# Performance work log

Measured on AMD Instinct MI355X. Metric: run time of the kernel, lower is better.

## Reference

```python
import jax, jax.numpy as jnp
from jax import lax
import numpy as np

SLOPE = 0.01   # torch nn.LeakyReLU default
EPS = 1e-5     # BN eps
DN = ('NCDHW', 'OIDHW', 'NCDHW')


def conv3d(x, w, pad):
    return lax.conv_general_dilated(x, w, (1, 1, 1), pad, dimension_numbers=DN)


def bn(x, g, b):
    # BatchNorm1d over all active points == per-channel stats over (N, D, H, W)
    m = jnp.mean(x, axis=(0, 2, 3, 4), keepdims=True)
    v = jnp.var(x, axis=(0, 2, 3, 4), keepdims=True)
    return (x - m) * lax.rsqrt(v + EPS) * g.reshape(1, -1, 1, 1, 1) + b.reshape(1, -1, 1, 1, 1)


def lrelu(x):
    return jnp.where(x >= 0, x, SLOPE * x)


def setup_inputs() -> dict:
    key = jax.random.key(0)
    ks = jax.random.split(key, 8)
    Cin, Cout = 128, 64
    x = jax.random.normal(ks[0], (1, Cin, 16, 48, 48), jnp.float32)      # coarse sparse grid (all-active)
    skip = jax.random.normal(ks[1], (1, Cout, 32, 96, 96), jnp.float32)  # fine skip grid
    s = lambda k, shape, fan: jax.random.normal(k, shape, jnp.float32) * np.float32(1.0 / np.sqrt(fan))
    w_trans = s(ks[2], (Cout, Cin, 3, 3, 3), Cin * 27)
    w_up = s(ks[3], (Cout, Cout, 3, 3, 3), Cout * 27)
    w1 = s(ks[4], (Cout, Cout, 1, 3, 3), Cout * 9)
    w2 = s(ks[5], (Cout, Cout, 3, 1, 3), Cout * 9)
    w3 = s(ks[6], (Cout, Cout, 3, 3, 3), Cout * 27)
    g = jnp.ones((Cout,), jnp.float32)
    b = jnp.zeros((Cout,), jnp.float32)
    return dict(x=x, skip=skip, w_trans=w_trans, g_t=g, b_t=b, w_up=w_up,
                w1=w1, g1=g, b1=b, w2=w2, g2=g, b2=b, w3=w3, g3=g, b3=b)


def reference(x, skip, w_trans, g_t, b_t, w_up, w1, g1, b1, w2, g2, b2, w3, g3, b3):
    # trans_conv (subm 3x3x3) -> LeakyReLU -> BN
    xt = bn(lrelu(conv3d(x, w_trans, [(1, 1)] * 3)), g_t, b_t)
    up = lax.conv_general_dilated(xt, w_up, (1, 1, 1), [(1, 2)] * 3,
                                  lhs_dilation=(2, 2, 2), dimension_numbers=DN)
    up = up + skip
    up = bn(lrelu(conv3d(up, w1, [(0, 0), (1, 1), (1, 1)])), g1, b1)  # conv1x3 (1,3,3)
    up = bn(lrelu(conv3d(up, w2, [(1, 1), (0, 0), (1, 1)])), g2, b2)  # conv3x1 (3,1,3)
    up = bn(lrelu(conv3d(up, w3, [(1, 1)] * 3)), g3, b3)              # conv3x3 (3,3,3)
    return up
```

## Files before the change

### kernel.cpp

```cpp
#include <hip/hip_runtime.h>

#define SLOPE 0.01f
#define BN_EPS 1e-5f

typedef __attribute__((ext_vector_type(8))) short short8;
typedef __attribute__((ext_vector_type(4))) float f32x4;

static constexpr int D1 = 32, H1 = 96, W1_ = 96;
static constexpr int HW1 = H1 * W1_, DHW1 = D1 * HW1;
static constexpr int D0 = 16, H0 = 48, W0 = 48;
static constexpr int HW0 = H0 * W0, DHW0 = D0 * HW0;

static constexpr int FP_PLPTS = 98 * 98;
static constexpr int CP_PLPTS = 50 * 50;
static constexpr int FP_ELEMS = 33 * FP_PLPTS * 64;

__device__ __forceinline__ short f2bf(float f) {
    unsigned u = __builtin_bit_cast(unsigned, f);
    unsigned r = (u + 0x7fffu + ((u >> 16) & 1u)) >> 16;
    return (short)r;
}
__device__ __forceinline__ float bf2f(short s) {
    unsigned u = ((unsigned)(unsigned short)s) << 16;
    return __builtin_bit_cast(float, u);
}
__device__ __forceinline__ int pidx_fine(int s) {
    int z = s / HW1; int r = s - z * HW1; int y = r / W1_; int x = r - y * W1_;
    return z * FP_PLPTS + (y + 1) * 98 + (x + 1);
}
__device__ __forceinline__ int pidx_coarse(int s) {
    int z = s / HW0; int r = s - z * HW0; int y = r / W0; int x = r - y * W0;
    return z * CP_PLPTS + (y + 1) * 50 + (x + 1);
}
__device__ __forceinline__ void gload16(const void* g, void* l) {
    __builtin_amdgcn_global_load_lds(
        (const __attribute__((address_space(1))) void*)g,
        (__attribute__((address_space(3))) void*)l, 16, 0, 0);
}

__global__ __launch_bounds__(256)
void to_cl_pad128(const float* __restrict__ in, short* __restrict__ out)
{
    __shared__ float t[64][65];
    const int s0 = blockIdx.x * 64, c0 = blockIdx.y * 64;
    const int tid = threadIdx.x;
    {
        const int cpr = tid >> 2, ch = tid & 3;
        const float4* ip = (const float4*)(in + (size_t)(c0 + cpr) * DHW0 + s0 + ch * 16);
        #pragma unroll
        for (int i = 0; i < 4; ++i) {
            float4 v = ip[i]; int sb = ch * 16 + i * 4;
            t[sb][cpr] = v.x; t[sb + 1][cpr] = v.y; t[sb + 2][cpr] = v.z; t[sb + 3][cpr] = v.w;
        }
    }
    __syncthreads();
    {
        const int spr = tid >> 2, cc = (tid & 3) * 16;
        short8 o0, o1;
        #pragma unroll
        for (int q = 0; q < 8; ++q) { o0[q] = f2bf(t[spr][cc + q]); o1[q] = f2bf(t[spr][cc + 8 + q]); }
        const int p = pidx_coarse(s0 + spr);
        short* op = out + (size_t)p * 128 + c0 + cc;
        *(short8*)op = o0;
        *(short8*)(op + 8) = o1;
    }
}

__global__ __launch_bounds__(256)
void to_cl_bf16(const float* __restrict__ in, short* __restrict__ out, int S)
{
    __shared__ float t[64][65];
    const int s0 = blockIdx.x * 64;
    const int tid = threadIdx.x;
    {
        const int cpr = tid >> 2, ch = tid & 3;
        const float4* ip = (const float4*)(in + (size_t)cpr * S + s0 + ch * 16);
        #pragma unroll
        for (int i = 0; i < 4; ++i) {
            float4 v = ip[i]; int sb = ch * 16 + i * 4;
            t[sb][cpr] = v.x; t[sb + 1][cpr] = v.y; t[sb + 2][cpr] = v.z; t[sb + 3][cpr] = v.w;
        }
    }
    __syncthreads();
    {
        const int spr = tid >> 2, cc = (tid & 3) * 16;
        short8 o0, o1;
        #pragma unroll
        for (int q = 0; q < 8; ++q) { o0[q] = f2bf(t[spr][cc + q]); o1[q] = f2bf(t[spr][cc + 8 + q]); }
        short* op = out + (size_t)(s0 + spr) * 64 + cc;
        *(short8*)op = o0;
        *(short8*)(op + 8) = o1;
    }
}

__global__ __launch_bounds__(256)
void prep_w(const float* __restrict__ w, short* __restrict__ dst, int CIN, int KSZ)
{
    int i = blockIdx.x * 256 + threadIdx.x;
    int n = KSZ * 64 * CIN;
    if (i >= n) return;
    int t = i / (64 * CIN); int r = i % (64 * CIN); int o = r / CIN; int ci = r % CIN;
    dst[i] = f2bf(w[(size_t)(o * CIN + ci) * KSZ + t]);
}

__global__ void finalize_stats(const float* __restrict__ stats, const float* __restrict__ g,
                               const float* __restrict__ b, float invN, float* __restrict__ aff)
{
    int c = threadIdx.x;
    float m = stats[c] * invN;
    float var = stats[64 + c] * invN - m * m;
    float rstd = rsqrtf(var + BN_EPS);
    float sc = g[c] * rstd;
    aff[c] = sc;
    aff[64 + c] = b[c] - m * sc;
}

template<int MODE>
__global__ __launch_bounds__(256)
void affine_pad(short* __restrict__ buf, const float* __restrict__ aff, int n8)
{
    int i = blockIdx.x * 256 + threadIdx.x;
    if (i >= n8) return;
    int s = i >> 3, cb = (i & 7) * 8;
    int p = (MODE == 1) ? pidx_fine(s) : pidx_coarse(s);
    short* ptr = buf + (size_t)p * 64 + cb;
    short8 v = *(const short8*)ptr;
    short8 o;
    #pragma unroll
    for (int q = 0; q < 8; ++q) {
        int c = cb + q;
        o[q] = f2bf(bf2f(v[q]) * aff[c] + aff[64 + c]);
    }
    *(short8*)ptr = o;
}

__global__ __launch_bounds__(256)
void final_out(const short* __restrict__ in, float* __restrict__ out, const float* __restrict__ aff)
{
    __shared__ float t[64][65];
    const int s0 = blockIdx.x * 64;
    const int tid = threadIdx.x;
    {
        const int spr = tid >> 2, ch = tid & 3;
        const short8* ip = (const short8*)(in + (size_t)(s0 + spr) * 64 + ch * 16);
        short8 v0 = ip[0], v1 = ip[1];
        #pragma unroll
        for (int q = 0; q < 8; ++q) { int c = ch * 16 + q;     t[spr][c] = bf2f(v0[q]) * aff[c] + aff[64 + c]; }
        #pragma unroll
        for (int q = 0; q < 8; ++q) { int c = ch * 16 + 8 + q; t[spr][c] = bf2f(v1[q]) * aff[c] + aff[64 + c]; }
    }
    __syncthreads();
    {
        const int c = tid >> 2, sc = (tid & 3) * 16;
        #pragma unroll
        for (int i = 0; i < 4; ++i) {
            float4 w;
            w.x = t[sc + 4 * i][c]; w.y = t[sc + 4 * i + 1][c];
            w.z = t[sc + 4 * i + 2][c]; w.w = t[sc + 4 * i + 3][c];
            *(float4*)(out + (size_t)c * DHW1 + s0 + sc + 4 * i) = w;
        }
    }
}

template<int GH, int GW, int CIN>
__global__ __launch_bounds__(256)
void zero_halo(short* __restrict__ buf)
{
    constexpr int PPW = GW + 2, PLP = (GH + 2) * PPW, CPR = CIN / 8;
    constexpr int NCHK = (2 * PPW + 2 * GH) * CPR;
    const int pl = blockIdx.x;
    const short8 z8 = {0, 0, 0, 0, 0, 0, 0, 0};
    for (int i = threadIdx.x; i < NCHK; i += 256) {
        int p = i / CPR, c = i % CPR;
        int y, x;
        if (p < PPW) { y = 0; x = p; }
        else if (p < 2 * PPW) { y = GH + 1; x = p - PPW; }
        else { int q = p - 2 * PPW; y = 1 + (q >> 1); x = (q & 1) ? (GW + 1) : 0; }
        *(short8*)(buf + ((size_t)pl * PLP + y * PPW + x) * CIN + c * 8) = z8;
    }
}

template<int MG, int CIN, int KD, int KH, int KW, int PD, int PH, int PW,
         int GD, int GH, int GW, int OUTMODE, bool STATS>
__global__ __launch_bounds__(256, 2)
void convmm5(const short* __restrict__ A, const short* __restrict__ Wt,
             short* __restrict__ Out, float* __restrict__ stats)
{
    constexpr int MR   = 64 * MG;
    constexpr int KSZ  = KD * KH * KW;
    constexpr int PPW  = GW + 2;
    constexpr int PLP  = (GH + 2) * PPW;
    constexpr int HWg  = GH * GW;
    constexpr int CPR  = CIN / 8;
    constexpr int L2C  = (CIN == 64) ? 3 : 4;
    constexpr int RPI  = 64 / CPR;
    constexpr int ASZ  = MR * CIN * 2;
    constexpr int BSZ  = 64 * CIN * 2;
    constexpr int API  = ASZ / 4096;
    constexpr int BPI  = BSZ / 4096;
    constexpr int KCN  = CIN / 32;
    constexpr int S_IF = API + BPI;

    __shared__ char smem[2 * ASZ + 2 * BSZ];

    const int tid = threadIdx.x, lane = tid & 63, wave = tid >> 6;
    const int rl = lane & 15, kg = lane >> 4;

    const int nwg = gridDim.x;
    const int bid = blockIdx.x;
    const int bswz = (nwg & 7) ? bid : ((bid & 7) * (nwg >> 3) + (bid >> 3));
    const int row0 = bswz * MR;

    int zA[API], yxA[API], cofA[API];
    #pragma unroll
    for (int i = 0; i < API; ++i) {
        const int gi = wave * API + i;
        const int r = gi * RPI + (lane >> L2C);
        const int s = row0 + r;
        const int z = s / HWg; const int rm = s - z * HWg;
        const int y = rm / GW; const int x = rm - y * GW;
        zA[i] = z;
        yxA[i] = (y + 1) * PPW + (x + 1);
        cofA[i] = ((lane & (CPR - 1)) ^ (r & 7)) * 8;
    }
    int rB[BPI], cofB[BPI];
    #pragma unroll
    for (int i = 0; i < BPI; ++i) {
        const int gi = wave * BPI + i;
        const int r = gi * RPI + (lane >> L2C);
        rB[i] = r;
        cofB[i] = ((lane & (CPR - 1)) ^ (r & 7)) * 8;
    }

    auto stageA = [&](int bsel, int kd, int kh, int kw) {
        const int dyx = (kh - PH) * PPW + (kw - PW);
        #pragma unroll
        for (int i = 0; i < API; ++i) {
            int zp = zA[i] + (kd - PD);
            int pl = ((unsigned)zp < (unsigned)GD) ? zp : GD;
            const short* src = A + ((size_t)pl * PLP + yxA[i] + dyx) * CIN + cofA[i];
            void* dst = smem + bsel * ASZ + (wave * API + i) * 1024;
            gload16(src, dst);
        }
    };
    auto stageB = [&](int bsel, int t) {
        const short* wt = Wt + (size_t)t * 64 * CIN;
        #pragma unroll
        for (int i = 0; i < BPI; ++i) {
            const short* src = wt + rB[i] * CIN + cofB[i];
            void* dst = smem + 2 * ASZ + bsel * BSZ + (wave * BPI + i) * 1024;
            gload16(src, dst);
        }
    };

    f32x4 acc[MG][4];
    #pragma unroll
    for (int mg = 0; mg < MG; ++mg)
        #pragma unroll
        for (int ng = 0; ng < 4; ++ng)
            acc[mg][ng] = (f32x4){0.f, 0.f, 0.f, 0.f};

    auto comp = [&](int bsel) {
        const short* ab = (const short*)(smem + bsel * ASZ);
        const short* bb = (const short*)(smem + 2 * ASZ + bsel * BSZ);
        #pragma unroll
        for (int kc = 0; kc < KCN; ++kc) {
            short8 av[MG], bv[4];
            #pragma unroll
            for (int mg = 0; mg < MG; ++mg) {
                const int r = wave * (16 * MG) + mg * 16 + rl;
                const int c = (kc * 4 + kg) ^ (r & 7);
                av[mg] = *(const short8*)(ab + r * CIN + c * 8);
            }
            #pragma unroll
            for (int ng = 0; ng < 4; ++ng) {
                const int r = ng * 16 + rl;
                const int c = (kc * 4 + kg) ^ (r & 7);
                bv[ng] = *(const short8*)(bb + r * CIN + c * 8);
            }
            __builtin_amdgcn_s_setprio(1);
            #pragma unroll
            for (int mg = 0; mg < MG; ++mg)
                #pragma unroll
                for (int ng = 0; ng < 4; ++ng)
                    acc[mg][ng] = __builtin_amdgcn_mfma_f32_16x16x32_bf16(av[mg], bv[ng], acc[mg][ng], 0, 0, 0);
            __builtin_amdgcn_s_setprio(0);
        }
    };

    stageA(0, 0, 0, 0);
    stageB(0, 0);

    #pragma unroll
    for (int t = 0; t < KSZ; ++t) {
        const int cur = t & 1;
        if (t + 1 < KSZ) {
            const int t1 = t + 1;
            const int kd = t1 / (KH * KW), rm = t1 % (KH * KW);
            stageA(cur ^ 1, kd, rm / KW, rm % KW);
            stageB(cur ^ 1, t1);
            asm volatile("s_waitcnt vmcnt(%0)" :: "i"(S_IF) : "memory");
        } else {
            asm volatile("s_waitcnt vmcnt(0)" ::: "memory");
        }
        __builtin_amdgcn_s_barrier();
        __builtin_amdgcn_sched_barrier(0);
        comp(cur);
        asm volatile("s_waitcnt lgkmcnt(0)" ::: "memory");
        __builtin_amdgcn_sched_barrier(0);
        __builtin_amdgcn_s_barrier();
    }

    short (*tile)[64] = (short(*)[64])smem;
    float* red = (float*)(smem + 2 * ASZ);

    #pragma unroll
    for (int mg = 0; mg < MG; ++mg)
        #pragma unroll
        for (int ng = 0; ng < 4; ++ng)
            #pragma unroll
            for (int j = 0; j < 4; ++j) {
                float v = acc[mg][ng][j];
                if (STATS) v = (v >= 0.f) ? v : SLOPE * v;
                tile[wave * (16 * MG) + mg * 16 + kg * 4 + j][ng * 16 + rl] = f2bf(v);
            }
    __syncthreads();

    #pragma unroll
    for (int i = 0; i < MR / 32; ++i) {
        const int chunk = i * 256 + tid;
        const int r = chunk >> 3, cc = (chunk & 7) * 8;
        const int s = row0 + r;
        size_t o;
        if (OUTMODE == 0)      o = (size_t)s * 64 + cc;
        else if (OUTMODE == 1) o = (size_t)pidx_fine(s) * 64 + cc;
        else                   o = (size_t)pidx_coarse(s) * 64 + cc;
        *(short8*)(Out + o) = *(const short8*)&tile[r][cc];
    }

    if (STATS) {
        float s1 = 0.f, s2 = 0.f;
        const int col = tid & 63, rg = tid >> 6;
        #pragma unroll 4
        for (int r = rg * (MR / 4); r < (rg + 1) * (MR / 4); ++r) {
            float v = bf2f(tile[r][col]); s1 += v; s2 += v * v;
        }
        red[(0 * 4 + rg) * 64 + col] = s1;
        red[(1 * 4 + rg) * 64 + col] = s2;
        __syncthreads();
        if (tid < 64) {
            float a = red[0 * 256 + 0 * 64 + tid] + red[0 * 256 + 1 * 64 + tid] +
                      red[0 * 256 + 2 * 64 + tid] + red[0 * 256 + 3 * 64 + tid];
            float b = red[1 * 256 + 0 * 64 + tid] + red[1 * 256 + 1 * 64 + tid] +
                      red[1 * 256 + 2 * 64 + tid] + red[1 * 256 + 3 * 64 + tid];
            atomicAdd(&stats[tid], a);
            atomicAdd(&stats[64 + tid], b);
        }
    }
}

__global__ __launch_bounds__(256, 2)
void tconv_cls(const short* __restrict__ Y, const short* __restrict__ Wt,
               const short* __restrict__ SK, short* __restrict__ Out)
{
    const int cls = blockIdx.y;
    const int pz = (cls >> 2) & 1, py = (cls >> 1) & 1, px = cls & 1;
    const int tid = threadIdx.x, lane = tid & 63, wave = tid >> 6;
    const int rl = lane & 15, kg = lane >> 4;
    const int row0 = blockIdx.x * 256;

    int zin0[4], zin1[4];
    #pragma unroll
    for (int mg = 0; mg < 4; ++mg) {
        int s = row0 + wave * 64 + mg * 16 + rl;
        int zc = s / HW0; int r = s - zc * HW0; int yc = r / W0; int xc = r - yc * W0;
        int ib = ((yc + 1) * 50 + (xc + 1)) * 64 + kg * 8;
        zin0[mg] = zc * (CP_PLPTS * 64) + ib;
        zin1[mg] = ((zc + 1 < 16) ? zc + 1 : 16) * (CP_PLPTS * 64) + ib;
    }
    const int boff = rl * 64 + kg * 8;

    f32x4 acc[4][4];
    #pragma unroll
    for (int mg = 0; mg < 4; ++mg)
        #pragma unroll
        for (int ng = 0; ng < 4; ++ng)
            acc[mg][ng] = (f32x4){0.f, 0.f, 0.f, 0.f};

    for (int a = 0; a <= pz; ++a) {
        const int kd = pz ? 2 * a : 1;
        for (int b = 0; b <= py; ++b) {
            const int kh = py ? 2 * b : 1;
            for (int c = 0; c <= px; ++c) {
                const int kw = px ? 2 * c : 1;
                const int t = kd * 9 + kh * 3 + kw;
                const int dlt = (b * 50 + c) * 64;
                int ao[4];
                #pragma unroll
                for (int mg = 0; mg < 4; ++mg)
                    ao[mg] = (a ? zin1[mg] : zin0[mg]) + dlt;
                #pragma unroll
                for (int kc = 0; kc < 2; ++kc) {
                    short8 av[4], bv[4];
                    #pragma unroll
                    for (int mg = 0; mg < 4; ++mg)
                        av[mg] = *(const short8*)(Y + ao[mg] + kc * 32);
                    #pragma unroll
                    for (int ng = 0; ng < 4; ++ng)
                        bv[ng] = *(const short8*)(Wt + (t * 64 + ng * 16) * 64 + boff + kc * 32);
                    #pragma unroll
                    for (int mg = 0; mg < 4; ++mg)
                        #pragma unroll
                        for (int ng = 0; ng < 4; ++ng)
                            acc[mg][ng] = __builtin_amdgcn_mfma_f32_16x16x32_bf16(av[mg], bv[ng], acc[mg][ng], 0, 0, 0);
                }
            }
        }
    }

    __shared__ short tile[256][72];
    #pragma unroll
    for (int mg = 0; mg < 4; ++mg)
        #pragma unroll
        for (int ng = 0; ng < 4; ++ng)
            #pragma unroll
            for (int j = 0; j < 4; ++j)
                tile[wave * 64 + mg * 16 + kg * 4 + j][ng * 16 + rl] = f2bf(acc[mg][ng][j]);
    __syncthreads();

    #pragma unroll
    for (int i = 0; i < 8; ++i) {
        int chunk = i * 256 + tid;
        int r = chunk >> 3, cc = (chunk & 7) * 8;
        int sl = row0 + r;
        int zc = sl / HW0; int rr = sl - zc * HW0; int yc = rr / W0; int xc = rr - yc * W0;
        int z = 2 * zc + pz, y = 2 * yc + py, x = 2 * xc + px;
        size_t so = (size_t)((z * H1 + y) * W1_ + x) * 64 + cc;
        size_t po = (size_t)(z * FP_PLPTS + (y + 1) * 98 + (x + 1)) * 64 + cc;
        short8 v = *(const short8*)&tile[r][cc];
        short8 skv = *(const short8*)(SK + so);
        short8 o;
        #pragma unroll
        for (int q = 0; q < 8; ++q) o[q] = f2bf(bf2f(v[q]) + bf2f(skv[q]));
        *(short8*)(Out + po) = o;
    }
}

extern "C" void kernel_launch(void* const* d_in, const int* in_sizes, int n_in,
                              void* d_out, int out_size, void* d_ws, size_t ws_size,
                              hipStream_t stream)
{
    const float* x       = (const float*)d_in[0];
    const float* skip    = (const float*)d_in[1];
    const float* w_trans = (const float*)d_in[2];
    const float* g_t     = (const float*)d_in[3];
    const float* b_t     = (const float*)d_in[4];
    const float* w_up    = (const float*)d_in[5];
    const float* w1      = (const float*)d_in[6];
    const float* g1      = (const float*)d_in[7];
    const float* b1      = (const float*)d_in[8];
    const float* w2      = (const float*)d_in[9];
    const float* g2      = (const float*)d_in[10];
    const float* b2      = (const float*)d_in[11];
    const float* w3      = (const float*)d_in[12];
    const float* g3      = (const float*)d_in[13];
    const float* b3      = (const float*)d_in[14];
    float* out = (float*)d_out;

    char* ws = (char*)d_ws;
    short* PadA = (short*)ws;
    short* PadB = (short*)(ws + (size_t)FP_ELEMS * 2);
    float* stats = (float*)(ws + (size_t)FP_ELEMS * 4);
    float* affs  = stats + 512;

    float* st0 = stats;       float* af0 = affs;
    float* st1 = stats + 128; float* af1 = affs + 128;
    float* st2 = stats + 256; float* af2 = affs + 256;
    float* st3 = stats + 384; float* af3 = affs + 384;

    char* ob = (char*)d_out;
    short* X0  = (short*)ob;
    short* Y0  = (short*)(ob + 10880000);
    short* SKb = (short*)(ob + 16320000);
    short* wt_t  = (short*)(ob + 54068736);
    short* wt_up = wt_t + 221184;
    short* wt_1  = wt_up + 110592;
    short* wt_2  = wt_1 + 36864;
    short* wt_3  = wt_2 + 36864;

    zero_halo<96, 96, 64><<<33, 256, 0, stream>>>(PadA);
    zero_halo<96, 96, 64><<<33, 256, 0, stream>>>(PadB);
    zero_halo<48, 48, 128><<<17, 256, 0, stream>>>(X0);
    zero_halo<48, 48, 64><<<17, 256, 0, stream>>>(Y0);
    hipMemsetAsync((char*)PadA + (size_t)32 * FP_PLPTS * 128, 0, FP_PLPTS * 128, stream);
    hipMemsetAsync((char*)PadB + (size_t)32 * FP_PLPTS * 128, 0, FP_PLPTS * 128, stream);
    hipMemsetAsync((char*)X0 + (size_t)16 * CP_PLPTS * 256, 0, CP_PLPTS * 256, stream);
    hipMemsetAsync((char*)Y0 + (size_t)16 * CP_PLPTS * 128, 0, CP_PLPTS * 128, stream);
    hipMemsetAsync(stats, 0, 2048, stream);

    prep_w<<<(27 * 64 * 128 + 255) / 256, 256, 0, stream>>>(w_trans, wt_t, 128, 27);
    prep_w<<<(27 * 64 * 64 + 255) / 256, 256, 0, stream>>>(w_up, wt_up, 64, 27);
    prep_w<<<(9 * 64 * 64 + 255) / 256, 256, 0, stream>>>(w1, wt_1, 64, 9);
    prep_w<<<(9 * 64 * 64 + 255) / 256, 256, 0, stream>>>(w2, wt_2, 64, 9);
    prep_w<<<(27 * 64 * 64 + 255) / 256, 256, 0, stream>>>(w3, wt_3, 64, 27);

    to_cl_pad128<<<dim3(DHW0 / 64, 2), 256, 0, stream>>>(x, X0);
    to_cl_bf16<<<DHW1 / 64, 256, 0, stream>>>(skip, SKb, DHW1);

    convmm5<1, 128, 3, 3, 3, 1, 1, 1, 16, 48, 48, 2, true>
        <<<DHW0 / 64, 256, 0, stream>>>(X0, wt_t, Y0, st0);
    finalize_stats<<<1, 64, 0, stream>>>(st0, g_t, b_t, 1.f / DHW0, af0);
    affine_pad<2><<<(DHW0 * 8 + 255) / 256, 256, 0, stream>>>(Y0, af0, DHW0 * 8);

    tconv_cls<<<dim3(DHW0 / 256, 8), 256, 0, stream>>>(Y0, wt_up, SKb, PadA);

    convmm5<4, 64, 1, 3, 3, 0, 1, 1, 32, 96, 96, 1, true>
        <<<DHW1 / 256, 256, 0, stream>>>(PadA, wt_1, PadB, st1);
    finalize_stats<<<1, 64, 0, stream>>>(st1, g1, b1, 1.f / DHW1, af1);
    affine_pad<1><<<(DHW1 * 8 + 255) / 256, 256, 0, stream>>>(PadB, af1, DHW1 * 8);

    convmm5<4, 64, 3, 1, 3, 1, 0, 1, 32, 96, 96, 1, true>
        <<<DHW1 / 256, 256, 0, stream>>>(PadB, wt_2, PadA, st2);
    finalize_stats<<<1, 64, 0, stream>>>(st2, g2, b2, 1.f / DHW1, af2);
    affine_pad<1><<<(DHW1 * 8 + 255) / 256, 256, 0, stream>>>(PadA, af2, DHW1 * 8);

    convmm5<4, 64, 3, 3, 3, 1, 1, 1, 32, 96, 96, 0, true>
        <<<DHW1 / 256, 256, 0, stream>>>(PadA, wt_3, PadB, st3);
    finalize_stats<<<1, 64, 0, stream>>>(st3, g3, b3, 1.f / DHW1, af3);

    final_out<<<DHW1 / 64, 256, 0, stream>>>(PadB, out, af3);
}
```

Baseline: 475.6 us.

## Stage contiguous padded row segment once per (kd,kh) and reuse across kw taps

The implicit-GEMM conv kernel now stages, for each (kd,kh) tap pair, one contiguous padded-row segment of input covering the tile plus a halo. The three kw taps then read shifted windows of that segment from LDS instead of restaging the A tile for every tap. Weights are no longer staged through LDS; each wave loads B fragments straight from global memory per kw. This cuts global-to-LDS traffic and barrier count by about a factor of three. In exchange, weight loads come from global or cache inside the compute loop, and the LDS read pattern for shifted rows is more irregular.

```diff
diff --git a/kernel.cpp b/kernel.cpp
--- a/kernel.cpp
+++ b/kernel.cpp
@@ -180,28 +180,25 @@
     }
 }
 
-template<int MG, int CIN, int KD, int KH, int KW, int PD, int PH, int PW,
+template<int MG, int CIN, int KD, int KH, int PD, int PH,
          int GD, int GH, int GW, int OUTMODE, bool STATS>
 __global__ __launch_bounds__(256, 2)
-void convmm5(const short* __restrict__ A, const short* __restrict__ Wt,
+void convmm6(const short* __restrict__ A, const short* __restrict__ Wt,
              short* __restrict__ Out, float* __restrict__ stats)
 {
     constexpr int MR   = 64 * MG;
-    constexpr int KSZ  = KD * KH * KW;
     constexpr int PPW  = GW + 2;
     constexpr int PLP  = (GH + 2) * PPW;
     constexpr int HWg  = GH * GW;
     constexpr int CPR  = CIN / 8;
-    constexpr int L2C  = (CIN == 64) ? 3 : 4;
-    constexpr int RPI  = 64 / CPR;
-    constexpr int ASZ  = MR * CIN * 2;
-    constexpr int BSZ  = 64 * CIN * 2;
-    constexpr int API  = ASZ / 4096;
-    constexpr int BPI  = BSZ / 4096;
     constexpr int KCN  = CIN / 32;
-    constexpr int S_IF = API + BPI;
-
-    __shared__ char smem[2 * ASZ + 2 * BSZ];
+    constexpr int LSEG = (MG == 4) ? 288 : 80;
+    constexpr int PPI  = 64 / CPR;
+    constexpr int API  = LSEG / (4 * PPI);
+    constexpr int ABYTES = LSEG * CIN * 2;
+    constexpr int P    = KD * KH;
+
+    __shared__ __align__(16) char smem[2 * ABYTES];
 
     const int tid = threadIdx.x, lane = tid & 63, wave = tid >> 6;
     const int rl = lane & 15, kg = lane >> 4;
@@ -209,46 +206,35 @@
     const int nwg = gridDim.x;
     const int bid = blockIdx.x;
     const int bswz = (nwg & 7) ? bid : ((bid & 7) * (nwg >> 3) + (bid >> 3));
-    const int row0 = bswz * MR;
-
-    int zA[API], yxA[API], cofA[API];
+    const int s0 = bswz * MR;
+    const int z0 = s0 / HWg;
+    const int rem0 = s0 - z0 * HWg;
+    const int yx0 = (rem0 / GW + 1) * PPW + (rem0 % GW + 1);
+
+    int jp_[API], cs_[API];
     #pragma unroll
     for (int i = 0; i < API; ++i) {
-        const int gi = wave * API + i;
-        const int r = gi * RPI + (lane >> L2C);
-        const int s = row0 + r;
-        const int z = s / HWg; const int rm = s - z * HWg;
-        const int y = rm / GW; const int x = rm - y * GW;
-        zA[i] = z;
-        yxA[i] = (y + 1) * PPW + (x + 1);
-        cofA[i] = ((lane & (CPR - 1)) ^ (r & 7)) * 8;
-    }
-    int rB[BPI], cofB[BPI];
-    #pragma unroll
-    for (int i = 0; i < BPI; ++i) {
-        const int gi = wave * BPI + i;
-        const int r = gi * RPI + (lane >> L2C);
-        rB[i] = r;
-        cofB[i] = ((lane & (CPR - 1)) ^ (r & 7)) * 8;
-    }
-
-    auto stageA = [&](int bsel, int kd, int kh, int kw) {
-        const int dyx = (kh - PH) * PPW + (kw - PW);
+        jp_[i] = (wave * API + i) * PPI + lane / CPR;
+        cs_[i] = (lane & (CPR - 1)) ^ (jp_[i] & 7);
+    }
+
+    int jm[MG];
+    #pragma unroll
+    for (int mg = 0; mg < MG; ++mg) {
+        int s = s0 + wave * (16 * MG) + mg * 16 + rl;
+        int rm = s - z0 * HWg;
+        jm[mg] = (rm / GW + 1) * PPW + (rm % GW + 1) - yx0;
+    }
+
+    auto stage = [&](int bsel, int kd, int kh) {
+        int zp = z0 + kd - PD;
+        size_t P0 = ((unsigned)zp < (unsigned)GD)
+            ? (size_t)zp * PLP + yx0 + (kh - PH) * PPW - 1
+            : (size_t)GD * PLP;
         #pragma unroll
         for (int i = 0; i < API; ++i) {
-            int zp = zA[i] + (kd - PD);
-            int pl = ((unsigned)zp < (unsigned)GD) ? zp : GD;
-            const short* src = A + ((size_t)pl * PLP + yxA[i] + dyx) * CIN + cofA[i];
-            void* dst = smem + bsel * ASZ + (wave * API + i) * 1024;
-            gload16(src, dst);
-        }
-    };
-    auto stageB = [&](int bsel, int t) {
-        const short* wt = Wt + (size_t)t * 64 * CIN;
-        #pragma unroll
-        for (int i = 0; i < BPI; ++i) {
-            const short* src = wt + rB[i] * CIN + cofB[i];
-            void* dst = smem + 2 * ASZ + bsel * BSZ + (wave * BPI + i) * 1024;
+            const short* src = A + (P0 + jp_[i]) * CIN + cs_[i] * 8;
+            void* dst = smem + bsel * ABYTES + (wave * API + i) * 1024 + lane * 16;
             gload16(src, dst);
         }
     };
@@ -260,59 +246,57 @@
         for (int ng = 0; ng < 4; ++ng)
             acc[mg][ng] = (f32x4){0.f, 0.f, 0.f, 0.f};
 
-    auto comp = [&](int bsel) {
-        const short* ab = (const short*)(smem + bsel * ASZ);
-        const short* bb = (const short*)(smem + 2 * ASZ + bsel * BSZ);
-        #pragma unroll
-        for (int kc = 0; kc < KCN; ++kc) {
-            short8 av[MG], bv[4];
+    auto comp = [&](int bsel, int T0) {
+        const char* ab = smem + bsel * ABYTES;
+        #pragma unroll
+        for (int kw = 0; kw < 3; ++kw) {
+            const short* wt = Wt + (size_t)(T0 + kw) * 64 * CIN;
+            short8 bv[KCN][4];
             #pragma unroll
-            for (int mg = 0; mg < MG; ++mg) {
-                const int r = wave * (16 * MG) + mg * 16 + rl;
-                const int c = (kc * 4 + kg) ^ (r & 7);
-                av[mg] = *(const short8*)(ab + r * CIN + c * 8);
-            }
-            #pragma unroll
-            for (int ng = 0; ng < 4; ++ng) {
-                const int r = ng * 16 + rl;
-                const int c = (kc * 4 + kg) ^ (r & 7);
-                bv[ng] = *(const short8*)(bb + r * CIN + c * 8);
-            }
-            __builtin_amdgcn_s_setprio(1);
-            #pragma unroll
-            for (int mg = 0; mg < MG; ++mg)
+            for (int kc = 0; kc < KCN; ++kc)
                 #pragma unroll
                 for (int ng = 0; ng < 4; ++ng)
-                    acc[mg][ng] = __builtin_amdgcn_mfma_f32_16x16x32_bf16(av[mg], bv[ng], acc[mg][ng], 0, 0, 0);
-            __builtin_amdgcn_s_setprio(0);
+                    bv[kc][ng] = *(const short8*)(wt + (ng * 16 + rl) * CIN + (kc * 4 + kg) * 8);
+            #pragma unroll
+            for (int kc = 0; kc < KCN; ++kc) {
+                short8 av[MG];
+                #pragma unroll
+                for (int mg = 0; mg < MG; ++mg) {
+                    const int j = jm[mg] + kw;
+                    av[mg] = *(const short8*)(ab + j * (CIN * 2) + (((kc * 4 + kg) ^ (j & 7)) << 4));
+                }
+                __builtin_amdgcn_s_setprio(1);
+                #pragma unroll
+                for (int mg = 0; mg < MG; ++mg)
+                    #pragma unroll
+                    for (int ng = 0; ng < 4; ++ng)
+                        acc[mg][ng] = __builtin_amdgcn_mfma_f32_16x16x32_bf16(av[mg], bv[kc][ng], acc[mg][ng], 0, 0, 0);
+                __builtin_amdgcn_s_setprio(0);
+            }
         }
     };
 
-    stageA(0, 0, 0, 0);
-    stageB(0, 0);
-
-    #pragma unroll
-    for (int t = 0; t < KSZ; ++t) {
-        const int cur = t & 1;
-        if (t + 1 < KSZ) {
-            const int t1 = t + 1;
-            const int kd = t1 / (KH * KW), rm = t1 % (KH * KW);
-            stageA(cur ^ 1, kd, rm / KW, rm % KW);
-            stageB(cur ^ 1, t1);
-            asm volatile("s_waitcnt vmcnt(%0)" :: "i"(S_IF) : "memory");
+    stage(0, 0, 0);
+
+    #pragma unroll
+    for (int p = 0; p < P; ++p) {
+        const int kd = p / KH, kh = p % KH;
+        if (p + 1 < P) {
+            stage((p + 1) & 1, (p + 1) / KH, (p + 1) % KH);
+            asm volatile("s_waitcnt vmcnt(%0)" :: "i"(API) : "memory");
         } else {
             asm volatile("s_waitcnt vmcnt(0)" ::: "memory");
         }
         __builtin_amdgcn_s_barrier();
         __builtin_amdgcn_sched_barrier(0);
-        comp(cur);
+        comp(p & 1, (kd * KH + kh) * 3);
         asm volatile("s_waitcnt lgkmcnt(0)" ::: "memory");
         __builtin_amdgcn_sched_barrier(0);
         __builtin_amdgcn_s_barrier();
     }
 
     short (*tile)[64] = (short(*)[64])smem;
-    float* red = (float*)(smem + 2 * ASZ);
+    float* red = (float*)(smem + ABYTES);
 
     #pragma unroll
     for (int mg = 0; mg < MG; ++mg)
@@ -330,7 +314,7 @@
     for (int i = 0; i < MR / 32; ++i) {
         const int chunk = i * 256 + tid;
         const int r = chunk >> 3, cc = (chunk & 7) * 8;
-        const int s = row0 + r;
+        const int s = s0 + r;
         size_t o;
         if (OUTMODE == 0)      o = (size_t)s * 64 + cc;
         else if (OUTMODE == 1) o = (size_t)pidx_fine(s) * 64 + cc;
@@ -345,14 +329,12 @@
         for (int r = rg * (MR / 4); r < (rg + 1) * (MR / 4); ++r) {
             float v = bf2f(tile[r][col]); s1 += v; s2 += v * v;
         }
-        red[(0 * 4 + rg) * 64 + col] = s1;
-        red[(1 * 4 + rg) * 64 + col] = s2;
+        red[rg * 64 + col] = s1;
+        red[256 + rg * 64 + col] = s2;
         __syncthreads();
         if (tid < 64) {
-            float a = red[0 * 256 + 0 * 64 + tid] + red[0 * 256 + 1 * 64 + tid] +
-                      red[0 * 256 + 2 * 64 + tid] + red[0 * 256 + 3 * 64 + tid];
-            float b = red[1 * 256 + 0 * 64 + tid] + red[1 * 256 + 1 * 64 + tid] +
-                      red[1 * 256 + 2 * 64 + tid] + red[1 * 256 + 3 * 64 + tid];
+            float a = red[tid] + red[64 + tid] + red[128 + tid] + red[192 + tid];
+            float b = red[256 + tid] + red[320 + tid] + red[384 + tid] + red[448 + tid];
             atomicAdd(&stats[tid], a);
             atomicAdd(&stats[64 + tid], b);
         }
@@ -471,12 +453,11 @@
     short* PadA = (short*)ws;
     short* PadB = (short*)(ws + (size_t)FP_ELEMS * 2);
     float* stats = (float*)(ws + (size_t)FP_ELEMS * 4);
-    float* affs  = stats + 512;
-
-    float* st0 = stats;       float* af0 = affs;
-    float* st1 = stats + 128; float* af1 = affs + 128;
-    float* st2 = stats + 256; float* af2 = affs + 256;
-    float* st3 = stats + 384; float* af3 = affs + 384;
+
+    float* st0 = stats;       float* af0 = stats + 512;
+    float* st1 = stats + 128; float* af1 = stats + 512 + 128;
+    float* st2 = stats + 256; float* af2 = stats + 512 + 256;
+    float* st3 = stats + 384; float* af3 = stats + 512 + 384;
 
     char* ob = (char*)d_out;
     short* X0  = (short*)ob;
@@ -507,24 +488,24 @@
     to_cl_pad128<<<dim3(DHW0 / 64, 2), 256, 0, stream>>>(x, X0);
     to_cl_bf16<<<DHW1 / 64, 256, 0, stream>>>(skip, SKb, DHW1);
 
-    convmm5<1, 128, 3, 3, 3, 1, 1, 1, 16, 48, 48, 2, true>
+    convmm6<1, 128, 3, 3, 1, 1, 16, 48, 48, 2, true>
         <<<DHW0 / 64, 256, 0, stream>>>(X0, wt_t, Y0, st0);
     finalize_stats<<<1, 64, 0, stream>>>(st0, g_t, b_t, 1.f / DHW0, af0);
     affine_pad<2><<<(DHW0 * 8 + 255) / 256, 256, 0, stream>>>(Y0, af0, DHW0 * 8);
 
     tconv_cls<<<dim3(DHW0 / 256, 8), 256, 0, stream>>>(Y0, wt_up, SKb, PadA);
 
-    convmm5<4, 64, 1, 3, 3, 0, 1, 1, 32, 96, 96, 1, true>
+    convmm6<4, 64, 1, 3, 0, 1, 32, 96, 96, 1, true>
         <<<DHW1 / 256, 256, 0, stream>>>(PadA, wt_1, PadB, st1);
     finalize_stats<<<1, 64, 0, stream>>>(st1, g1, b1, 1.f / DHW1, af1);
     affine_pad<1><<<(DHW1 * 8 + 255) / 256, 256, 0, stream>>>(PadB, af1, DHW1 * 8);
 
-    convmm5<4, 64, 3, 1, 3, 1, 0, 1, 32, 96, 96, 1, true>
+    convmm6<4, 64, 3, 1, 1, 0, 32, 96, 96, 1, true>
         <<<DHW1 / 256, 256, 0, stream>>>(PadB, wt_2, PadA, st2);
     finalize_stats<<<1, 64, 0, stream>>>(st2, g2, b2, 1.f / DHW1, af2);
     affine_pad<1><<<(DHW1 * 8 + 255) / 256, 256, 0, stream>>>(PadA, af2, DHW1 * 8);
 
-    convmm5<4, 64, 3, 3, 3, 1, 1, 1, 32, 96, 96, 0, true>
+    convmm6<4, 64, 3, 3, 1, 1, 32, 96, 96, 0, true>
         <<<DHW1 / 256, 256, 0, stream>>>(PadA, wt_3, PadB, st3);
     finalize_stats<<<1, 64, 0, stream>>>(st3, g3, b3, 1.f / DHW1, af3);
 
```

Result: slower. 622.7 us (+30.9%).

## Add plane-row-staged convmm7 for fine convs and merge setup kernels

Applied to the files above, without the earlier changes.

Introduces a new conv kernel for the three fine-grid convolutions. It stages two padded output rows of input (208 points) once per (kd,kh) tap group and reuses them across the three kw taps by shifting the LDS row index. Weight tiles are double-buffered with explicit vmcnt waits, and the kernel uses 128 threads, 192 output rows per block and 6x4 MFMA accumulators per wave. It also merges the four halo-zeroing launches, the memsets and the five weight-prep launches into two kernels to cut launch overhead. The risks are lower occupancy from launch_bounds(128,1) and more register pressure.

```diff
diff --git a/kernel.cpp b/kernel.cpp
--- a/kernel.cpp
+++ b/kernel.cpp
@@ -93,14 +93,24 @@
     }
 }
 
-__global__ __launch_bounds__(256)
-void prep_w(const float* __restrict__ w, short* __restrict__ dst, int CIN, int KSZ)
-{
-    int i = blockIdx.x * 256 + threadIdx.x;
-    int n = KSZ * 64 * CIN;
-    if (i >= n) return;
+__device__ __forceinline__ void rp(const float* __restrict__ w, short* __restrict__ dst,
+                                   int CIN, int KSZ, int i)
+{
     int t = i / (64 * CIN); int r = i % (64 * CIN); int o = r / CIN; int ci = r % CIN;
     dst[i] = f2bf(w[(size_t)(o * CIN + ci) * KSZ + t]);
+}
+__global__ __launch_bounds__(256)
+void prep_all(const float* __restrict__ wt, const float* __restrict__ wu,
+              const float* __restrict__ w1, const float* __restrict__ w2,
+              const float* __restrict__ w3, short* dt, short* du,
+              short* d1, short* d2, short* d3)
+{
+    int i = blockIdx.x * 256 + threadIdx.x;
+    if (i < 221184) { rp(wt, dt, 128, 27, i); return; } i -= 221184;
+    if (i < 110592) { rp(wu, du, 64, 27, i); return; } i -= 110592;
+    if (i < 36864)  { rp(w1, d1, 64, 9, i);  return; } i -= 36864;
+    if (i < 36864)  { rp(w2, d2, 64, 9, i);  return; } i -= 36864;
+    if (i < 110592) rp(w3, d3, 64, 27, i);
 }
 
 __global__ void finalize_stats(const float* __restrict__ stats, const float* __restrict__ g,
@@ -162,22 +172,50 @@
     }
 }
 
-template<int GH, int GW, int CIN>
 __global__ __launch_bounds__(256)
-void zero_halo(short* __restrict__ buf)
-{
-    constexpr int PPW = GW + 2, PLP = (GH + 2) * PPW, CPR = CIN / 8;
-    constexpr int NCHK = (2 * PPW + 2 * GH) * CPR;
-    const int pl = blockIdx.x;
+void zero_misc(short* __restrict__ PadA, short* __restrict__ PadB,
+               short* __restrict__ X0, short* __restrict__ Y0, float* __restrict__ stats)
+{
     const short8 z8 = {0, 0, 0, 0, 0, 0, 0, 0};
-    for (int i = threadIdx.x; i < NCHK; i += 256) {
-        int p = i / CPR, c = i % CPR;
-        int y, x;
-        if (p < PPW) { y = 0; x = p; }
-        else if (p < 2 * PPW) { y = GH + 1; x = p - PPW; }
-        else { int q = p - 2 * PPW; y = 1 + (q >> 1); x = (q & 1) ? (GW + 1) : 0; }
-        *(short8*)(buf + ((size_t)pl * PLP + y * PPW + x) * CIN + c * 8) = z8;
-    }
+    int i = blockIdx.x * 256 + threadIdx.x;
+    constexpr int T_F = 33 * 3104 + 76832;
+    constexpr int T_X = 17 * 3136 + 40000;
+    constexpr int T_Y = 17 * 1568 + 20000;
+    constexpr int TOT = 2 * T_F + T_X + T_Y + 128;
+    if (i >= TOT) return;
+
+    auto fine_off = [](int q) -> size_t {
+        if (q < 33 * 3104) {
+            int pl = q / 3104, e = q % 3104, p = e >> 3, c = e & 7;
+            int y, x;
+            if (p < 98) { y = 0; x = p; }
+            else if (p < 196) { y = 97; x = p - 98; }
+            else { int q2 = p - 196; y = 1 + (q2 >> 1); x = (q2 & 1) ? 97 : 0; }
+            return ((size_t)pl * FP_PLPTS + y * 98 + x) * 64 + c * 8;
+        }
+        int q2 = q - 33 * 3104;
+        return (size_t)32 * FP_PLPTS * 64 + (size_t)q2 * 8;
+    };
+    auto co_off = [](int q, int CPR) -> size_t {
+        const int EPP = 196 * CPR;
+        if (q < 17 * EPP) {
+            int pl = q / EPP, e = q % EPP, p = e / CPR, c = e % CPR;
+            int y, x;
+            if (p < 50) { y = 0; x = p; }
+            else if (p < 100) { y = 49; x = p - 50; }
+            else { int r = p - 100; y = 1 + (r >> 1); x = (r & 1) ? 49 : 0; }
+            return ((size_t)pl * CP_PLPTS + y * 50 + x) * (CPR * 8) + c * 8;
+        }
+        int q2 = q - 17 * EPP;
+        return (size_t)16 * CP_PLPTS * (CPR * 8) + (size_t)q2 * 8;
+    };
+
+    if (i < T_F) { *(short8*)(PadA + fine_off(i)) = z8; return; } i -= T_F;
+    if (i < T_F) { *(short8*)(PadB + fine_off(i)) = z8; return; } i -= T_F;
+    if (i < T_X) { *(short8*)(X0 + co_off(i, 16)) = z8; return; } i -= T_X;
+    if (i < T_Y) { *(short8*)(Y0 + co_off(i, 8)) = z8; return; } i -= T_Y;
+    float4 zf = {0.f, 0.f, 0.f, 0.f};
+    *(float4*)((char*)stats + (size_t)i * 16) = zf;
 }
 
 template<int MG, int CIN, int KD, int KH, int KW, int PD, int PH, int PW,
@@ -345,16 +383,157 @@
         for (int r = rg * (MR / 4); r < (rg + 1) * (MR / 4); ++r) {
             float v = bf2f(tile[r][col]); s1 += v; s2 += v * v;
         }
-        red[(0 * 4 + rg) * 64 + col] = s1;
-        red[(1 * 4 + rg) * 64 + col] = s2;
+        red[rg * 64 + col] = s1;
+        red[256 + rg * 64 + col] = s2;
         __syncthreads();
         if (tid < 64) {
-            float a = red[0 * 256 + 0 * 64 + tid] + red[0 * 256 + 1 * 64 + tid] +
-                      red[0 * 256 + 2 * 64 + tid] + red[0 * 256 + 3 * 64 + tid];
-            float b = red[1 * 256 + 0 * 64 + tid] + red[1 * 256 + 1 * 64 + tid] +
-                      red[1 * 256 + 2 * 64 + tid] + red[1 * 256 + 3 * 64 + tid];
+            float a = red[tid] + red[64 + tid] + red[128 + tid] + red[192 + tid];
+            float b = red[256 + tid] + red[320 + tid] + red[384 + tid] + red[448 + tid];
             atomicAdd(&stats[tid], a);
             atomicAdd(&stats[64 + tid], b);
+        }
+    }
+}
+
+template<int KD, int KH, int PD, int PH, int OUTMODE, bool STATS>
+__global__ __launch_bounds__(128, 1)
+void convmm7(const short* __restrict__ A, const short* __restrict__ Wt,
+             short* __restrict__ Out, float* __restrict__ stats)
+{
+    constexpr int KSZ = KD * KH * 3, NG = KD * KH;
+    constexpr int PLP = FP_PLPTS;
+    constexpr int ABYTES = 208 * 128;
+    constexpr int BBYTES = 8192;
+    __shared__ __align__(16) char smem[2 * ABYTES + 2 * BBYTES];
+
+    const int tid = threadIdx.x, lane = tid & 63, wave = tid >> 6;
+    const int rl = lane & 15, kg = lane >> 4;
+
+    const int nwg = gridDim.x, bid = blockIdx.x;
+    const int bswz = (bid & 7) * (nwg >> 3) + (bid >> 3);
+    const int s0 = bswz * 192;
+    const int z0 = s0 / HW1;
+    const int y0 = (s0 - z0 * HW1) / 96;
+
+    const int ptl = lane >> 3;
+    const int csl = (lane & 7) ^ ptl;
+
+    auto stageA = [&](int bsel, int g) {
+        const int kd = g / KH, kh = g % KH;
+        const int zp = z0 + kd - PD;
+        const int pl = ((unsigned)zp < 32u) ? zp : 32;
+        const int ys = y0 + kh - PH;
+        const size_t base = (size_t)pl * PLP + (size_t)(ys + 1) * 98;
+        #pragma unroll
+        for (int i = 0; i < 13; ++i) {
+            const int ii = wave * 13 + i;
+            const short* src = A + (base + ii * 8 + ptl) * 64 + csl * 8;
+            gload16(src, smem + bsel * ABYTES + ii * 1024);
+        }
+    };
+    auto stageB = [&](int bsel, int t) {
+        const short* wt = Wt + (size_t)t * 4096;
+        #pragma unroll
+        for (int i = 0; i < 4; ++i) {
+            const int ii = wave * 4 + i;
+            const short* src = wt + (ii * 8 + ptl) * 64 + csl * 8;
+            gload16(src, smem + 2 * ABYTES + bsel * BBYTES + ii * 1024);
+        }
+    };
+
+    f32x4 acc[6][4];
+    #pragma unroll
+    for (int mg = 0; mg < 6; ++mg)
+        #pragma unroll
+        for (int ng = 0; ng < 4; ++ng)
+            acc[mg][ng] = (f32x4){0.f, 0.f, 0.f, 0.f};
+
+    const int jb = wave * 98 + rl;
+
+    stageA(0, 0);
+    stageB(0, 0);
+
+    #pragma unroll
+    for (int t = 0; t < KSZ; ++t) {
+        const int g = t / 3, kw = t % 3;
+        if (kw == 0 && g + 1 < NG) stageA((g + 1) & 1, g + 1);
+        if (t + 1 < KSZ) stageB((t + 1) & 1, t + 1);
+        if (t == KSZ - 1)
+            asm volatile("s_waitcnt vmcnt(0)" ::: "memory");
+        else if (kw == 0 && g + 1 < NG)
+            asm volatile("s_waitcnt vmcnt(17)" ::: "memory");
+        else
+            asm volatile("s_waitcnt vmcnt(4)" ::: "memory");
+        __builtin_amdgcn_s_barrier();
+        __builtin_amdgcn_sched_barrier(0);
+
+        const char* ab = smem + (g & 1) * ABYTES;
+        const char* bb = smem + 2 * ABYTES + (t & 1) * BBYTES;
+        #pragma unroll
+        for (int kc = 0; kc < 2; ++kc) {
+            short8 bv[4], av[6];
+            #pragma unroll
+            for (int ng = 0; ng < 4; ++ng) {
+                const int row = ng * 16 + rl;
+                bv[ng] = *(const short8*)(bb + row * 128 + (((kc * 4 + kg) ^ (rl & 7)) << 4));
+            }
+            #pragma unroll
+            for (int mg = 0; mg < 6; ++mg) {
+                const int j = jb + mg * 16 + kw;
+                av[mg] = *(const short8*)(ab + j * 128 + (((kc * 4 + kg) ^ (j & 7)) << 4));
+            }
+            __builtin_amdgcn_s_setprio(1);
+            #pragma unroll
+            for (int mg = 0; mg < 6; ++mg)
+                #pragma unroll
+                for (int ng = 0; ng < 4; ++ng)
+                    acc[mg][ng] = __builtin_amdgcn_mfma_f32_16x16x32_bf16(av[mg], bv[ng], acc[mg][ng], 0, 0, 0);
+            __builtin_amdgcn_s_setprio(0);
+        }
+        asm volatile("s_waitcnt lgkmcnt(0)" ::: "memory");
+        __builtin_amdgcn_sched_barrier(0);
+        __builtin_amdgcn_s_barrier();
+    }
+
+    short (*tile)[64] = (short(*)[64])smem;
+    float* red = (float*)(smem + 192 * 64 * 2);
+
+    #pragma unroll
+    for (int mg = 0; mg < 6; ++mg)
+        #pragma unroll
+        for (int ng = 0; ng < 4; ++ng)
+            #pragma unroll
+            for (int j = 0; j < 4; ++j) {
+                float v = acc[mg][ng][j];
+                if (STATS) v = (v >= 0.f) ? v : SLOPE * v;
+                tile[wave * 96 + mg * 16 + kg * 4 + j][ng * 16 + rl] = f2bf(v);
+            }
+    __syncthreads();
+
+    #pragma unroll
+    for (int i = 0; i < 12; ++i) {
+        const int chunk = i * 128 + tid;
+        const int r = chunk >> 3, cc = (chunk & 7) * 8;
+        const int s = s0 + r;
+        size_t o;
+        if (OUTMODE == 0) o = (size_t)s * 64 + cc;
+        else              o = (size_t)pidx_fine(s) * 64 + cc;
+        *(short8*)(Out + o) = *(const short8*)&tile[r][cc];
+    }
+
+    if (STATS) {
+        float s1 = 0.f, s2 = 0.f;
+        const int col = tid & 63, rg = tid >> 6;
+        #pragma unroll 4
+        for (int r = rg * 96; r < rg * 96 + 96; ++r) {
+            float v = bf2f(tile[r][col]); s1 += v; s2 += v * v;
+        }
+        red[rg * 64 + col] = s1;
+        red[128 + rg * 64 + col] = s2;
+        __syncthreads();
+        if (tid < 64) {
+            atomicAdd(&stats[tid], red[tid] + red[64 + tid]);
+            atomicAdd(&stats[64 + tid], red[128 + tid] + red[192 + tid]);
         }
     }
 }
@@ -471,12 +650,11 @@
     short* PadA = (short*)ws;
     short* PadB = (short*)(ws + (size_t)FP_ELEMS * 2);
     float* stats = (float*)(ws + (size_t)FP_ELEMS * 4);
-    float* affs  = stats + 512;
-
-    float* st0 = stats;       float* af0 = affs;
-    float* st1 = stats + 128; float* af1 = affs + 128;
-    float* st2 = stats + 256; float* af2 = affs + 256;
-    float* st3 = stats + 384; float* af3 = affs + 384;
+
+    float* st0 = stats;       float* af0 = stats + 512;
+    float* st1 = stats + 128; float* af1 = stats + 512 + 128;
+    float* st2 = stats + 256; float* af2 = stats + 512 + 256;
+    float* st3 = stats + 384; float* af3 = stats + 512 + 384;
 
     char* ob = (char*)d_out;
     short* X0  = (short*)ob;
@@ -488,21 +666,11 @@
     short* wt_2  = wt_1 + 36864;
     short* wt_3  = wt_2 + 36864;
 
-    zero_halo<96, 96, 64><<<33, 256, 0, stream>>>(PadA);
-    zero_halo<96, 96, 64><<<33, 256, 0, stream>>>(PadB);
-    zero_halo<48, 48, 128><<<17, 256, 0, stream>>>(X0);
-    zero_halo<48, 48, 64><<<17, 256, 0, stream>>>(Y0);
-    hipMemsetAsync((char*)PadA + (size_t)32 * FP_PLPTS * 128, 0, FP_PLPTS * 128, stream);
-    hipMemsetAsync((char*)PadB + (size_t)32 * FP_PLPTS * 128, 0, FP_PLPTS * 128, stream);
-    hipMemsetAsync((char*)X0 + (size_t)16 * CP_PLPTS * 256, 0, CP_PLPTS * 256, stream);
-    hipMemsetAsync((char*)Y0 + (size_t)16 * CP_PLPTS * 128, 0, CP_PLPTS * 128, stream);
-    hipMemsetAsync(stats, 0, 2048, stream);
-
-    prep_w<<<(27 * 64 * 128 + 255) / 256, 256, 0, stream>>>(w_trans, wt_t, 128, 27);
-    prep_w<<<(27 * 64 * 64 + 255) / 256, 256, 0, stream>>>(w_up, wt_up, 64, 27);
-    prep_w<<<(9 * 64 * 64 + 255) / 256, 256, 0, stream>>>(w1, wt_1, 64, 9);
-    prep_w<<<(9 * 64 * 64 + 255) / 256, 256, 0, stream>>>(w2, wt_2, 64, 9);
-    prep_w<<<(27 * 64 * 64 + 255) / 256, 256, 0, stream>>>(w3, wt_3, 64, 27);
+    zero_misc<<<(2 * (33 * 3104 + 76832) + (17 * 3136 + 40000) + (17 * 1568 + 20000) + 128 + 255) / 256,
+               256, 0, stream>>>(PadA, PadB, X0, Y0, stats);
+
+    prep_all<<<2016, 256, 0, stream>>>(w_trans, w_up, w1, w2, w3,
+                                       wt_t, wt_up, wt_1, wt_2, wt_3);
 
     to_cl_pad128<<<dim3(DHW0 / 64, 2), 256, 0, stream>>>(x, X0);
     to_cl_bf16<<<DHW1 / 64, 256, 0, stream>>>(skip, SKb, DHW1);
@@ -514,18 +682,18 @@
 
     tconv_cls<<<dim3(DHW0 / 256, 8), 256, 0, stream>>>(Y0, wt_up, SKb, PadA);
 
-    convmm5<4, 64, 1, 3, 3, 0, 1, 1, 32, 96, 96, 1, true>
-        <<<DHW1 / 256, 256, 0, stream>>>(PadA, wt_1, PadB, st1);
+    convmm7<1, 3, 0, 1, 1, true>
+        <<<DHW1 / 192, 128, 0, stream>>>(PadA, wt_1, PadB, st1);
     finalize_stats<<<1, 64, 0, stream>>>(st1, g1, b1, 1.f / DHW1, af1);
     affine_pad<1><<<(DHW1 * 8 + 255) / 256, 256, 0, stream>>>(PadB, af1, DHW1 * 8);
 
-    convmm5<4, 64, 3, 1, 3, 1, 0, 1, 32, 96, 96, 1, true>
-        <<<DHW1 / 256, 256, 0, stream>>>(PadB, wt_2, PadA, st2);
+    convmm7<3, 1, 1, 0, 1, true>
+        <<<DHW1 / 192, 128, 0, stream>>>(PadB, wt_2, PadA, st2);
     finalize_stats<<<1, 64, 0, stream>>>(st2, g2, b2, 1.f / DHW1, af2);
     affine_pad<1><<<(DHW1 * 8 + 255) / 256, 256, 0, stream>>>(PadA, af2, DHW1 * 8);
 
-    convmm5<4, 64, 3, 3, 3, 1, 1, 1, 32, 96, 96, 0, true>
-        <<<DHW1 / 256, 256, 0, stream>>>(PadA, wt_3, PadB, st3);
+    convmm7<3, 3, 1, 1, 0, true>
+        <<<DHW1 / 192, 128, 0, stream>>>(PadA, wt_3, PadB, st3);
     finalize_stats<<<1, 64, 0, stream>>>(st3, g3, b3, 1.f / DHW1, af3);
 
     final_out<<<DHW1 / 64, 256, 0, stream>>>(PadB, out, af3);
```

New measurement: 410.2 us. 1.16x faster.
